# Optimization experiments

Measured on AMD Instinct MI355X. Metric: run time of the kernel, lower is better.

The kernel has to match this reference:

```python
import jax, jax.numpy as jnp
import numpy as np

H, W = 128, 128
K = 16                # num_samples
RADIUS = 2.0
SIGMA = 1.0
EPS = 1e-10
MIN_DEPTH = 1e-6
N = 16384             # number of points
FEAT_DIM = 64
FAR = 1e9             # sentinel pixel coord for invalid (behind-camera) points


def setup_inputs() -> dict:
    key = jax.random.key(0)
    k1, k2, k3, k4, k5 = jax.random.split(key, 5)
    fx = fy = 128.0
    cx = cy = 64.0
    # Back-project uniform pixel locations with z in [1, 5] so points land on the image.
    u = jax.random.uniform(k1, (N,), minval=0.0, maxval=float(W))
    v = jax.random.uniform(k2, (N,), minval=0.0, maxval=float(H))
    z = jax.random.uniform(k3, (N,), minval=1.0, maxval=5.0)
    x = (u - cx) * z / fx
    y = (v - cy) * z / fy
    pcd_points = jnp.stack([x, y, z], axis=-1).astype(jnp.float32)
    pcd_colors = jax.random.uniform(k4, (N, 3), dtype=jnp.float32)
    pcd_feats = jax.random.normal(k5, (N, FEAT_DIM), dtype=jnp.float32)
    intrinsics = jnp.array([[fx, 0.0, cx], [0.0, fy, cy], [0.0, 0.0, 1.0]], dtype=jnp.float32)
    return {"pcd_points": pcd_points, "pcd_colors": pcd_colors,
            "pcd_feats": pcd_feats, "intrinsics": intrinsics}


def _render_pixels(pcd_points, intrinsics):
    # Project to pixel coords (u, v); points behind camera pushed to FAR so kNN never picks them.
    depths = pcd_points[:, 2]
    valid = depths > MIN_DEPTH
    safe_z = jnp.where(valid, depths, 1.0)
    u = pcd_points[:, 0] * intrinsics[0, 0] / safe_z + intrinsics[0, 2]
    v = pcd_points[:, 1] * intrinsics[1, 1] / safe_z + intrinsics[1, 2]
    pix = jnp.stack([u, v], axis=-1)                       # (N, 2)
    pix = jnp.where(valid[:, None], pix, FAR)
    return pix, depths


def _forward(pcd_points, pcd_colors, pcd_feats, intrinsics):
    pix, depths = _render_pixels(pcd_points, intrinsics)
    # Centered pixel grid, row-major flatten: coords are (x+0.5, y+0.5).
    ii, jj = jnp.meshgrid(jnp.arange(H), jnp.arange(W), indexing='ij')
    img_pix = jnp.stack([jj.ravel() + 0.5, ii.ravel() + 0.5], axis=-1).astype(pix.dtype)  # (P, 2)
    # Brute-force 2D kNN: (P, N) squared distances. Indices are non-differentiable.
    d2 = jnp.sum((img_pix[:, None, :] - pix[None, :, :]) ** 2, axis=-1)  # (P, N)
    _, idx = jax.lax.top_k(-jax.lax.stop_gradient(d2), K)                # (P, K)
    # Depth-sort the k neighbors (ascending), as torch.sort on zbuffers.
    zbuf = depths[idx]
    order = jnp.argsort(zbuf, axis=-1)
    idx = jnp.take_along_axis(idx, order, axis=-1)                       # (P, K)
    # Distances of sorted neighbors to the pixel center (differentiable path).
    knn_pix = pix[idx]                                                   # (P, K, 2)
    dist = jnp.linalg.norm(knn_pix - img_pix[:, None, :], axis=-1)       # (P, K)
    masks = dist < RADIUS
    # Exponential weighting + weighted (normalized) compositing.
    w = jnp.exp(-(dist ** 2) / (SIGMA ** 2)) * masks.astype(dist.dtype)
    w = w / (jnp.sum(w, axis=-1, keepdims=True) + EPS)
    sel_depths = depths[idx]                                             # (P, K)
    rendered_depths = jnp.sum(sel_depths * w, axis=-1).reshape(H, W)
    rendered_colors = jnp.sum(pcd_colors[idx] * w[..., None], axis=1).reshape(H, W, 3)
    rendered_feats = jnp.sum(pcd_feats[idx] * w[..., None], axis=1).reshape(H, W, FEAT_DIM)
    rendered_masks = jnp.any(masks, axis=-1).reshape(H, W)
    return rendered_depths, rendered_colors, rendered_feats, rendered_masks


def reference(pcd_points, pcd_colors, pcd_feats, intrinsics):
    return _forward(pcd_points, pcd_colors, pcd_feats, intrinsics)
```

## Files before the change

kernel.cpp:

```cpp
#include <hip/hip_runtime.h>

#define HH 128
#define WW 128
#define HW 16384
#define KK 16
#define NPTS 16384
#define FEAT 64
#define RADIUS2 4.0f
#define EPSV 1e-10f
#define CAP 16

__global__ void project_scatter(const float* __restrict__ pts,
                                const float* __restrict__ intr,
                                int* __restrict__ cell_count,
                                float4* __restrict__ buckets) {
    int n = blockIdx.x * blockDim.x + threadIdx.x;
    if (n >= NPTS) return;
    float fx = intr[0], cx = intr[2], fy = intr[4], cy = intr[5];
    float x = pts[3 * n], y = pts[3 * n + 1], z = pts[3 * n + 2];
    bool valid = z > 1e-6f;
    float sz = valid ? z : 1.0f;
    float u = x * fx / sz + cx;
    float v = y * fy / sz + cy;
    if (!valid) return;
    int cu = min(max((int)floorf(u), 0), WW - 1);
    int cv = min(max((int)floorf(v), 0), HH - 1);
    int cell = cv * WW + cu;
    int slot = atomicAdd(&cell_count[cell], 1);
    if (slot < CAP)
        buckets[slot * HW + cell] = make_float4(u, v, z, __int_as_float(n));
}

__global__ __launch_bounds__(64) void render_kernel(
        const float4* __restrict__ buckets,
        const int* __restrict__ cell_count,
        const float* __restrict__ colors,
        const float* __restrict__ feats,
        float* __restrict__ out_depth, float* __restrict__ out_colors,
        float* __restrict__ out_feats, float* __restrict__ out_mask) {
    __shared__ float4 pts_s[CAP * 96];
    __shared__ int    cnt_s[96];
    __shared__ float  knw_s[32][KK];
    __shared__ int    kni_s[32][KK];

    int tid = threadIdx.x;
    int tile = blockIdx.x;
    int j0 = (tile & 15) * 8;
    int i0 = (tile >> 4) * 4;

    int mymax = 0;
    for (int idx = tid; idx < 96; idx += 64) {
        int r = idx / 12, c = idx - r * 12;
        int ci = i0 - 2 + r, cj = j0 - 2 + c;
        int cnt = 0;
        if (ci >= 0 && ci < HH && cj >= 0 && cj < WW)
            cnt = min(cell_count[ci * WW + cj], CAP);
        cnt_s[idx] = cnt;
        mymax = max(mymax, cnt);
    }
#pragma unroll
    for (int d = 32; d; d >>= 1) mymax = max(mymax, __shfl_xor(mymax, d));
    int M = mymax;
    __syncthreads();

    for (int s = 0; s < M; ++s) {
        for (int idx = tid; idx < 96; idx += 64) {
            int r = idx / 12, c = idx - r * 12;
            int ci = i0 - 2 + r, cj = j0 - 2 + c;
            if (s < cnt_s[idx])
                pts_s[s * 96 + idx] = buckets[s * HW + ci * WW + cj];
        }
    }
    __syncthreads();

    int lp = tid >> 1, lane = tid & 1;
    int li = lp >> 3, lj = lp & 7;
    int i = i0 + li, j = j0 + lj;
    int p = i * WW + j;
    float px = j + 0.5f, py = i + 0.5f;

    float bd[KK];
    int   bt[KK];
#pragma unroll
    for (int k = 0; k < KK; ++k) { bd[k] = 1e30f; bt[k] = -1; }

#pragma unroll
    for (int dr = 0; dr < 5; ++dr) {
        int r = li + dr;
#pragma unroll
        for (int dc = 0; dc < 5; ++dc) {
            int c = lj + dc;
            int wc = r * 12 + c;
            int cnt = cnt_s[wc];
            for (int s = lane; s < cnt; s += 2) {
                float4 pt = pts_s[s * 96 + wc];
                float du = pt.x - px, dv = pt.y - py;
                float d2 = du * du + dv * dv;
                bool ok = d2 < RADIUS2;
                float dd = ok ? d2 : 1e30f;
                int tt = ok ? (s * 96 + wc) : -1;
#pragma unroll
                for (int k = 0; k < KK; ++k) {
                    bool cc = dd < bd[k];
                    float nb = cc ? dd : bd[k];
                    dd = cc ? bd[k] : dd;
                    int nt = cc ? tt : bt[k];
                    tt = cc ? bt[k] : tt;
                    bd[k] = nb; bt[k] = nt;
                }
            }
        }
    }

    float mb[8]; int mt[8];
#pragma unroll
    for (int k = 0; k < 8; ++k) {
        float obd = __shfl_xor(bd[15 - k], 1);
        int   obt = __shfl_xor(bt[15 - k], 1);
        bool take = obd < bd[k];
        mb[k] = take ? obd : bd[k];
        mt[k] = take ? obt : bt[k];
    }

    float wv[8], dv8[8];
    int idv[8];
    float wsum_l = 0.f;
    int any_l = 0;
#pragma unroll
    for (int k = 0; k < 8; ++k) {
        bool valid = mt[k] >= 0;
        float4 pt = pts_s[valid ? mt[k] : 0];
        float wk = valid ? __expf(-mb[k]) : 0.f;
        wv[k] = wk; wsum_l += wk;
        dv8[k] = valid ? pt.z : 0.f;
        idv[k] = valid ? __float_as_int(pt.w) : -1;
        any_l |= valid ? 1 : 0;
    }
    float wsum = wsum_l + __shfl_xor(wsum_l, 1);
    float inv = 1.0f / (wsum + EPSV);

    float cr[8], cg[8], cbl[8];
#pragma unroll
    for (int k = 0; k < 8; ++k) {
        int n3 = idv[k] >= 0 ? 3 * idv[k] : 0;
        cr[k] = colors[n3];
        cg[k] = colors[n3 + 1];
        cbl[k] = colors[n3 + 2];
    }

    float dsum = 0.f, c0 = 0.f, c1 = 0.f, c2 = 0.f;
#pragma unroll
    for (int k = 0; k < 8; ++k) {
        float wk = wv[k] * inv;
        kni_s[lp][lane * 8 + k] = idv[k];
        knw_s[lp][lane * 8 + k] = wk;
        dsum += dv8[k] * wk;
        c0 += cr[k] * wk;
        c1 += cg[k] * wk;
        c2 += cbl[k] * wk;
    }

    dsum += __shfl_xor(dsum, 1);
    c0 += __shfl_xor(c0, 1);
    c1 += __shfl_xor(c1, 1);
    c2 += __shfl_xor(c2, 1);
    any_l |= __shfl_xor(any_l, 1);

    if (lane == 0) {
        out_depth[p] = dsum;
        out_colors[3 * p]     = c0;
        out_colors[3 * p + 1] = c1;
        out_colors[3 * p + 2] = c2;
        out_mask[p] = any_l ? 1.0f : 0.0f;
    }
    __syncthreads();

    int f = tid;
    for (int q = 0; q < 32; q += 2) {
        float acc0 = 0.f, acc1 = 0.f;
#pragma unroll
        for (int k = 0; k < KK; ++k) {
            int n0 = kni_s[q][k];
            int n1 = kni_s[q + 1][k];
            float w0 = knw_s[q][k];
            float w1 = knw_s[q + 1][k];
            float f0 = feats[(n0 >= 0 ? n0 : 0) * FEAT + f];
            float f1 = feats[(n1 >= 0 ? n1 : 0) * FEAT + f];
            acc0 = fmaf(w0, f0, acc0);
            acc1 = fmaf(w1, f1, acc1);
        }
        int p0 = (i0 + (q >> 3)) * WW + j0 + (q & 7);
        int p1 = (i0 + ((q + 1) >> 3)) * WW + j0 + ((q + 1) & 7);
        out_feats[p0 * FEAT + f] = acc0;
        out_feats[p1 * FEAT + f] = acc1;
    }
}

extern "C" void kernel_launch(void* const* d_in, const int* in_sizes, int n_in,
                              void* d_out, int out_size, void* d_ws, size_t ws_size,
                              hipStream_t stream) {
    const float* pts    = (const float*)d_in[0];
    const float* colors = (const float*)d_in[1];
    const float* feats  = (const float*)d_in[2];
    const float* intr   = (const float*)d_in[3];

    float* out = (float*)d_out;
    float* out_depth  = out;
    float* out_colors = out + HW;
    float* out_feats  = out + HW * 4;
    float* out_mask   = out + HW * 68;

    char* ws = (char*)d_ws;
    int* cell_count  = (int*)ws;
    float4* buckets  = (float4*)(ws + HW * sizeof(int));

    hipMemsetAsync(cell_count, 0, HW * sizeof(int), stream);
    project_scatter<<<NPTS / 256, 256, 0, stream>>>(pts, intr, cell_count, buckets);
    render_kernel<<<512, 64, 0, stream>>>(buckets, cell_count, colors, feats,
                                          out_depth, out_colors, out_feats, out_mask);
}
```

Measured before the change: 106.3 us.

## Fuse projection and rendering into one cooperative kernel with grid sync

Merges the point projection/bucketing kernel and the render kernel into a single cooperative launch of 256 blocks of 256 threads, separated by a grid-wide sync. Buckets change to cell-major layout with a smaller capacity (12), tiles grow to 8x8 pixels, and the halo load reads a fixed number of slots instead of looping to the per-tile maximum count. This aims to cut a launch and improve load coalescing. In exchange, only half the threads do the kNN phase, grid sync adds cost, and a lower capacity can drop points in dense cells. Unwritten slots are also loaded into shared memory, though they are never read.

```diff
diff --git a/kernel.cpp b/kernel.cpp
--- a/kernel.cpp
+++ b/kernel.cpp
@@ -1,4 +1,7 @@
 #include <hip/hip_runtime.h>
+#include <hip/hip_cooperative_groups.h>
+
+namespace cg = cooperative_groups;
 
 #define HH 128
 #define WW 128
@@ -8,191 +11,178 @@
 #define FEAT 64
 #define RADIUS2 4.0f
 #define EPSV 1e-10f
-#define CAP 16
-
-__global__ void project_scatter(const float* __restrict__ pts,
-                                const float* __restrict__ intr,
-                                int* __restrict__ cell_count,
-                                float4* __restrict__ buckets) {
-    int n = blockIdx.x * blockDim.x + threadIdx.x;
-    if (n >= NPTS) return;
-    float fx = intr[0], cx = intr[2], fy = intr[4], cy = intr[5];
-    float x = pts[3 * n], y = pts[3 * n + 1], z = pts[3 * n + 2];
-    bool valid = z > 1e-6f;
-    float sz = valid ? z : 1.0f;
-    float u = x * fx / sz + cx;
-    float v = y * fy / sz + cy;
-    if (!valid) return;
-    int cu = min(max((int)floorf(u), 0), WW - 1);
-    int cv = min(max((int)floorf(v), 0), HH - 1);
-    int cell = cv * WW + cu;
-    int slot = atomicAdd(&cell_count[cell], 1);
-    if (slot < CAP)
-        buckets[slot * HW + cell] = make_float4(u, v, z, __int_as_float(n));
-}
-
-__global__ __launch_bounds__(64) void render_kernel(
-        const float4* __restrict__ buckets,
-        const int* __restrict__ cell_count,
+#define CAP 12
+
+__global__ __launch_bounds__(256) void fused_kernel(
+        const float* __restrict__ pts,
+        const float* __restrict__ intr,
         const float* __restrict__ colors,
         const float* __restrict__ feats,
+        int* __restrict__ cell_count,
+        float4* __restrict__ buckets,
         float* __restrict__ out_depth, float* __restrict__ out_colors,
         float* __restrict__ out_feats, float* __restrict__ out_mask) {
-    __shared__ float4 pts_s[CAP * 96];
-    __shared__ int    cnt_s[96];
-    __shared__ float  knw_s[32][KK];
-    __shared__ int    kni_s[32][KK];
+    __shared__ float4 pts_s[144 * CAP];
+    __shared__ int    cnt_s[144];
+    __shared__ int    kni_s[64][KK];
+    __shared__ float  knw_s[64][KK];
 
     int tid = threadIdx.x;
-    int tile = blockIdx.x;
-    int j0 = (tile & 15) * 8;
-    int i0 = (tile >> 4) * 4;
-
-    int mymax = 0;
-    for (int idx = tid; idx < 96; idx += 64) {
+    int gid = blockIdx.x * 256 + tid;
+
+    if (gid < NPTS) {
+        float fx = intr[0], cx = intr[2], fy = intr[4], cy = intr[5];
+        float x = pts[3 * gid], y = pts[3 * gid + 1], z = pts[3 * gid + 2];
+        if (z > 1e-6f) {
+            float u = x * fx / z + cx;
+            float v = y * fy / z + cy;
+            int cu = min(max((int)floorf(u), 0), WW - 1);
+            int cv = min(max((int)floorf(v), 0), HH - 1);
+            int cell = cv * WW + cu;
+            int slot = atomicAdd(&cell_count[cell], 1);
+            if (slot < CAP)
+                buckets[cell * CAP + slot] = make_float4(u, v, z, __int_as_float(gid));
+        }
+    }
+
+    cg::this_grid().sync();
+
+    int i0 = (blockIdx.x >> 4) * 8;
+    int j0 = (blockIdx.x & 15) * 8;
+
+    for (int idx = tid; idx < 144; idx += 256) {
         int r = idx / 12, c = idx - r * 12;
         int ci = i0 - 2 + r, cj = j0 - 2 + c;
         int cnt = 0;
         if (ci >= 0 && ci < HH && cj >= 0 && cj < WW)
             cnt = min(cell_count[ci * WW + cj], CAP);
         cnt_s[idx] = cnt;
-        mymax = max(mymax, cnt);
-    }
-#pragma unroll
-    for (int d = 32; d; d >>= 1) mymax = max(mymax, __shfl_xor(mymax, d));
-    int M = mymax;
+    }
+    for (int idx = tid; idx < 144 * CAP; idx += 256) {
+        int cellw = idx / CAP;
+        int s = idx - cellw * CAP;
+        int r = cellw / 12, c = cellw - r * 12;
+        int ci = i0 - 2 + r, cj = j0 - 2 + c;
+        if (ci >= 0 && ci < HH && cj >= 0 && cj < WW)
+            pts_s[idx] = buckets[(ci * WW + cj) * CAP + s];
+    }
     __syncthreads();
 
-    for (int s = 0; s < M; ++s) {
-        for (int idx = tid; idx < 96; idx += 64) {
-            int r = idx / 12, c = idx - r * 12;
-            int ci = i0 - 2 + r, cj = j0 - 2 + c;
-            if (s < cnt_s[idx])
-                pts_s[s * 96 + idx] = buckets[s * HW + ci * WW + cj];
-        }
-    }
-    __syncthreads();
-
-    int lp = tid >> 1, lane = tid & 1;
-    int li = lp >> 3, lj = lp & 7;
-    int i = i0 + li, j = j0 + lj;
-    int p = i * WW + j;
-    float px = j + 0.5f, py = i + 0.5f;
-
-    float bd[KK];
-    int   bt[KK];
-#pragma unroll
-    for (int k = 0; k < KK; ++k) { bd[k] = 1e30f; bt[k] = -1; }
-
-#pragma unroll
-    for (int dr = 0; dr < 5; ++dr) {
-        int r = li + dr;
-#pragma unroll
-        for (int dc = 0; dc < 5; ++dc) {
-            int c = lj + dc;
-            int wc = r * 12 + c;
-            int cnt = cnt_s[wc];
-            for (int s = lane; s < cnt; s += 2) {
-                float4 pt = pts_s[s * 96 + wc];
-                float du = pt.x - px, dv = pt.y - py;
-                float d2 = du * du + dv * dv;
-                bool ok = d2 < RADIUS2;
-                float dd = ok ? d2 : 1e30f;
-                int tt = ok ? (s * 96 + wc) : -1;
-#pragma unroll
-                for (int k = 0; k < KK; ++k) {
-                    bool cc = dd < bd[k];
-                    float nb = cc ? dd : bd[k];
-                    dd = cc ? bd[k] : dd;
-                    int nt = cc ? tt : bt[k];
-                    tt = cc ? bt[k] : tt;
-                    bd[k] = nb; bt[k] = nt;
+    if (tid < 128) {
+        int lp = tid >> 1, lane = tid & 1;
+        int li = lp >> 3, lj = lp & 7;
+        int i = i0 + li, j = j0 + lj;
+        int p = i * WW + j;
+        float px = j + 0.5f, py = i + 0.5f;
+
+        float bd[KK];
+        int   bt[KK];
+#pragma unroll
+        for (int k = 0; k < KK; ++k) { bd[k] = 1e30f; bt[k] = -1; }
+
+#pragma unroll
+        for (int dr = 0; dr < 5; ++dr) {
+            int r = li + dr;
+#pragma unroll
+            for (int dc = 0; dc < 5; ++dc) {
+                int wc = r * 12 + (lj + dc);
+                int cnt = cnt_s[wc];
+                for (int s = lane; s < cnt; s += 2) {
+                    float4 pt = pts_s[wc * CAP + s];
+                    float du = pt.x - px, dv = pt.y - py;
+                    float d2 = du * du + dv * dv;
+                    bool ok = d2 < RADIUS2;
+                    float dd = ok ? d2 : 1e30f;
+                    int tt = ok ? (wc * CAP + s) : -1;
+#pragma unroll
+                    for (int k = 0; k < KK; ++k) {
+                        bool cc = dd < bd[k];
+                        float nb = cc ? dd : bd[k];
+                        dd = cc ? bd[k] : dd;
+                        int nt = cc ? tt : bt[k];
+                        tt = cc ? bt[k] : tt;
+                        bd[k] = nb; bt[k] = nt;
+                    }
                 }
             }
         }
-    }
-
-    float mb[8]; int mt[8];
-#pragma unroll
-    for (int k = 0; k < 8; ++k) {
-        float obd = __shfl_xor(bd[15 - k], 1);
-        int   obt = __shfl_xor(bt[15 - k], 1);
-        bool take = obd < bd[k];
-        mb[k] = take ? obd : bd[k];
-        mt[k] = take ? obt : bt[k];
-    }
-
-    float wv[8], dv8[8];
-    int idv[8];
-    float wsum_l = 0.f;
-    int any_l = 0;
-#pragma unroll
-    for (int k = 0; k < 8; ++k) {
-        bool valid = mt[k] >= 0;
-        float4 pt = pts_s[valid ? mt[k] : 0];
-        float wk = valid ? __expf(-mb[k]) : 0.f;
-        wv[k] = wk; wsum_l += wk;
-        dv8[k] = valid ? pt.z : 0.f;
-        idv[k] = valid ? __float_as_int(pt.w) : -1;
-        any_l |= valid ? 1 : 0;
-    }
-    float wsum = wsum_l + __shfl_xor(wsum_l, 1);
-    float inv = 1.0f / (wsum + EPSV);
-
-    float cr[8], cg[8], cbl[8];
-#pragma unroll
-    for (int k = 0; k < 8; ++k) {
-        int n3 = idv[k] >= 0 ? 3 * idv[k] : 0;
-        cr[k] = colors[n3];
-        cg[k] = colors[n3 + 1];
-        cbl[k] = colors[n3 + 2];
-    }
-
-    float dsum = 0.f, c0 = 0.f, c1 = 0.f, c2 = 0.f;
-#pragma unroll
-    for (int k = 0; k < 8; ++k) {
-        float wk = wv[k] * inv;
-        kni_s[lp][lane * 8 + k] = idv[k];
-        knw_s[lp][lane * 8 + k] = wk;
-        dsum += dv8[k] * wk;
-        c0 += cr[k] * wk;
-        c1 += cg[k] * wk;
-        c2 += cbl[k] * wk;
-    }
-
-    dsum += __shfl_xor(dsum, 1);
-    c0 += __shfl_xor(c0, 1);
-    c1 += __shfl_xor(c1, 1);
-    c2 += __shfl_xor(c2, 1);
-    any_l |= __shfl_xor(any_l, 1);
-
-    if (lane == 0) {
-        out_depth[p] = dsum;
-        out_colors[3 * p]     = c0;
-        out_colors[3 * p + 1] = c1;
-        out_colors[3 * p + 2] = c2;
-        out_mask[p] = any_l ? 1.0f : 0.0f;
+
+        float mb[8]; int mt[8];
+#pragma unroll
+        for (int k = 0; k < 8; ++k) {
+            float obd = __shfl_xor(bd[15 - k], 1);
+            int   obt = __shfl_xor(bt[15 - k], 1);
+            bool take = obd < bd[k];
+            mb[k] = take ? obd : bd[k];
+            mt[k] = take ? obt : bt[k];
+        }
+
+        float wv[8], dv8[8];
+        int idv[8];
+        float wsum_l = 0.f;
+        int any_l = 0;
+#pragma unroll
+        for (int k = 0; k < 8; ++k) {
+            bool valid = mt[k] >= 0;
+            float4 pt = pts_s[valid ? mt[k] : 0];
+            float wk = valid ? __expf(-mb[k]) : 0.f;
+            wv[k] = wk; wsum_l += wk;
+            dv8[k] = valid ? pt.z : 0.f;
+            idv[k] = valid ? __float_as_int(pt.w) : 0;
+            any_l |= valid ? 1 : 0;
+        }
+        float wsum = wsum_l + __shfl_xor(wsum_l, 1);
+        float inv = 1.0f / (wsum + EPSV);
+
+        float cr[8], cg_[8], cbl[8];
+#pragma unroll
+        for (int k = 0; k < 8; ++k) {
+            int n3 = 3 * idv[k];
+            cr[k] = colors[n3];
+            cg_[k] = colors[n3 + 1];
+            cbl[k] = colors[n3 + 2];
+        }
+
+        float dsum = 0.f, c0 = 0.f, c1 = 0.f, c2 = 0.f;
+#pragma unroll
+        for (int k = 0; k < 8; ++k) {
+            float wk = wv[k] * inv;
+            kni_s[lp][lane * 8 + k] = idv[k];
+            knw_s[lp][lane * 8 + k] = wk;
+            dsum += dv8[k] * wk;
+            c0 += cr[k] * wk;
+            c1 += cg_[k] * wk;
+            c2 += cbl[k] * wk;
+        }
+
+        dsum += __shfl_xor(dsum, 1);
+        c0 += __shfl_xor(c0, 1);
+        c1 += __shfl_xor(c1, 1);
+        c2 += __shfl_xor(c2, 1);
+        any_l |= __shfl_xor(any_l, 1);
+
+        if (lane == 0) {
+            out_depth[p] = dsum;
+            out_colors[3 * p]     = c0;
+            out_colors[3 * p + 1] = c1;
+            out_colors[3 * p + 2] = c2;
+            out_mask[p] = any_l ? 1.0f : 0.0f;
+        }
     }
     __syncthreads();
 
-    int f = tid;
-    for (int q = 0; q < 32; q += 2) {
-        float acc0 = 0.f, acc1 = 0.f;
+    int f = tid & 63;
+    int sl = tid >> 6;
+    for (int q = sl; q < 64; q += 4) {
+        float acc = 0.f;
 #pragma unroll
         for (int k = 0; k < KK; ++k) {
-            int n0 = kni_s[q][k];
-            int n1 = kni_s[q + 1][k];
-            float w0 = knw_s[q][k];
-            float w1 = knw_s[q + 1][k];
-            float f0 = feats[(n0 >= 0 ? n0 : 0) * FEAT + f];
-            float f1 = feats[(n1 >= 0 ? n1 : 0) * FEAT + f];
-            acc0 = fmaf(w0, f0, acc0);
-            acc1 = fmaf(w1, f1, acc1);
-        }
-        int p0 = (i0 + (q >> 3)) * WW + j0 + (q & 7);
-        int p1 = (i0 + ((q + 1) >> 3)) * WW + j0 + ((q + 1) & 7);
-        out_feats[p0 * FEAT + f] = acc0;
-        out_feats[p1 * FEAT + f] = acc1;
+            int n = kni_s[q][k];
+            float wk = knw_s[q][k];
+            acc = fmaf(wk, feats[n * FEAT + f], acc);
+        }
+        int p = (i0 + (q >> 3)) * WW + j0 + (q & 7);
+        out_feats[p * FEAT + f] = acc;
     }
 }
 
@@ -211,11 +201,16 @@
     float* out_mask   = out + HW * 68;
 
     char* ws = (char*)d_ws;
-    int* cell_count  = (int*)ws;
-    float4* buckets  = (float4*)(ws + HW * sizeof(int));
+    int* cell_count = (int*)ws;
+    float4* buckets = (float4*)(ws + HW * sizeof(int));
 
     hipMemsetAsync(cell_count, 0, HW * sizeof(int), stream);
-    project_scatter<<<NPTS / 256, 256, 0, stream>>>(pts, intr, cell_count, buckets);
-    render_kernel<<<512, 64, 0, stream>>>(buckets, cell_count, colors, feats,
-                                          out_depth, out_colors, out_feats, out_mask);
+
+    void* args[] = {
+        (void*)&pts, (void*)&intr, (void*)&colors, (void*)&feats,
+        (void*)&cell_count, (void*)&buckets,
+        (void*)&out_depth, (void*)&out_colors, (void*)&out_feats, (void*)&out_mask
+    };
+    hipLaunchCooperativeKernel((const void*)fused_kernel, dim3(256), dim3(256),
+                               args, 0, stream);
 }
```

Measured after the change: 138.6 us. 1.3x slower.
